# Optimization experiments

Measured on AMD Instinct MI355X. Metric: run time of the kernel, lower is better.

## Reference

```python
import jax, jax.numpy as jnp
import numpy as np

B, C, D, Hh, W = 2, 320, 4, 16, 16
N = D * Hh * W          # 1024 nodes
NH = 8                  # num_heads
DH = C // NH            # 40
L = 2                   # num_layers
A, EPD = 16, 64         # da_prior tokens, encode_prior_dim
EDGE_SCALE = 32 ** -0.5 # GraphEdgeFeature dim_head=32
SCALE = DH ** -0.5
EPS = 1e-5


def _ln(x, g, b):
    m = x.mean(-1, keepdims=True)
    v = ((x - m) ** 2).mean(-1, keepdims=True)
    return (x - m) * jax.lax.rsqrt(v + EPS) * g + b


def setup_inputs() -> dict:
    key = jax.random.key(0)
    ks = jax.random.split(key, 16)
    std = 0.02 / np.sqrt(L)
    inp = {
        'x': jax.random.normal(ks[0], (B, C, D, Hh, W), jnp.float32),
        'da_prior': jax.random.normal(ks[1], (B, A, EPD), jnp.float32),
        # GraphEdgeFeature.to_qk (no bias), init std 0.02/sqrt(24)
        'qk_w': jax.random.normal(ks[2], (2 * C, C), jnp.float32) * (0.02 / np.sqrt(24)),
        # fc_prior
        'fcp_w': jax.random.normal(ks[3], (C, EPD), jnp.float32) * 0.02,
        'fcp_b': jnp.zeros((C,), jnp.float32),
        # per-layer (stacked over L)
        'ln1_g': jnp.ones((L, C), jnp.float32),
        'ln1_b': jnp.zeros((L, C), jnp.float32),
        'gln_g': jnp.ones((L, C), jnp.float32),
        'gln_b': jnp.zeros((L, C), jnp.float32),
        'qkv_w': jax.random.normal(ks[4], (L, 3 * C, C), jnp.float32) * std,
        'qkv_b': jnp.zeros((L, 3 * C), jnp.float32),
        'proj_w': jax.random.normal(ks[5], (L, C, C), jnp.float32) * std,
        'proj_b': jnp.zeros((L, C), jnp.float32),
        # expand Conv2d(1, NH, 1): weight [NH], bias [NH]
        'exp_w': jax.random.normal(ks[6], (L, NH), jnp.float32),
        'exp_b': jnp.zeros((L, NH), jnp.float32),
        # reduce Conv2d(NH, 1, 1): weight [NH], bias scalar
        'red_w': jax.random.normal(ks[7], (L, NH), jnp.float32) / np.sqrt(NH),
        'red_b': jnp.zeros((L,), jnp.float32),
    }
    return inp


def _forward(x, da_prior, qk_w, fcp_w, fcp_b, ln1_g, ln1_b, gln_g, gln_b,
             qkv_w, qkv_b, proj_w, proj_b, exp_w, exp_b, red_w, red_b):
    node = x.reshape(B, C, N)                       # [B,C,N]
    # ---- GraphEdgeFeature: full-dim QK attention over nodes ----
    xt = node.transpose(0, 2, 1)                    # [B,N,C]
    qk = xt @ qk_w.T                                # [B,N,2C]
    q_e, k_e = jnp.split(qk, 2, axis=-1)
    edge = jax.nn.softmax(jnp.einsum('bqc,bkc->bqk', q_e, k_e) * EDGE_SCALE, axis=-1)  # [B,N,N]
    # ---- fc_prior ----
    da = da_prior @ fcp_w.T + fcp_b                 # [B,A,C]
    s = da.sum(axis=1)                              # [B,C] (sum over 'a' in einsum bnc,bca->bnc)
    for l in range(L):
        # block norm1 over channel dim
        nt = _ln(node.transpose(0, 2, 1), ln1_g[l], ln1_b[l])   # [B,N,C]
        # torch.einsum('bnn,bnc->bnc') takes the DIAGONAL of edge
        diag = jnp.diagonal(edge, axis1=1, axis2=2)             # [B,N]
        node2 = diag[:, :, None] * nt * s[:, None, :] + nt      # [B,N,C]
        y = _ln(node2, gln_g[l], gln_b[l])
        qkv = (y @ qkv_w[l].T + qkv_b[l]).reshape(B, N, 3, NH, DH)
        qkv = qkv.transpose(2, 0, 3, 1, 4)                      # [3,B,H,N,DH]
        q, k, v = qkv[0], qkv[1], qkv[2]
        attn = jnp.einsum('bhnd,bhmd->bhnm', q, k) * SCALE
        attn = attn + edge[:, None] * exp_w[l][None, :, None, None] + exp_b[l][None, :, None, None]
        a = jax.nn.softmax(attn, axis=-1)                       # [B,H,N,N]
        node_out = jnp.einsum('bhnm,bhmd->bhnd', a, v).transpose(0, 2, 1, 3).reshape(B, N, C)
        edge_new = jnp.einsum('bhnm,h->bnm', a + attn, red_w[l]) + red_b[l]  # [B,N,N]
        ws = jax.nn.softmax(edge_new, axis=-1)
        wsum = (ws * edge_new).sum(-1)                          # [B,N]
        node_out = node_out + wsum[:, :, None]                  # fc=Identity, broadcast
        node_out = node_out @ proj_w[l].T + proj_b[l]
        node = node_out.transpose(0, 2, 1)                      # [B,C,N]
        edge = edge + edge_new
    return node.reshape(B, C, D, Hh, W)


def reference(x, da_prior, qk_w, fcp_w, fcp_b, ln1_g, ln1_b, gln_g, gln_b,
              qkv_w, qkv_b, proj_w, proj_b, exp_w, exp_b, red_w, red_b):
    return _forward(x, da_prior, qk_w, fcp_w, fcp_b, ln1_g, ln1_b, gln_g, gln_b,
                    qkv_w, qkv_b, proj_w, proj_b, exp_w, exp_b, red_w, red_b)
```

## Files before the change

kernel.cpp:

```cpp
#include <hip/hip_runtime.h>
#include <math.h>

#define EDGE_SCALE 0.17677669529663687f
#define ATT_SCALE  0.15811388300841897f
#define LN_EPS 1e-5f

typedef __attribute__((ext_vector_type(8))) short bf8;
typedef __attribute__((ext_vector_type(4))) float f32x4;

__device__ __forceinline__ f32x4 mfma16(bf8 a, bf8 b, f32x4 c) {
  return __builtin_amdgcn_mfma_f32_16x16x32_bf16(a, b, c, 0, 0, 0);
}
__device__ __forceinline__ unsigned short f2bf(float f) {
  union { float f; unsigned u; } v; v.f = f;
  unsigned r = v.u + 0x7FFF + ((v.u >> 16) & 1);
  return (unsigned short)(r >> 16);
}
__device__ __forceinline__ float bf2f(unsigned short h) {
  union { unsigned u; float f; } v; v.u = ((unsigned)h) << 16;
  return v.f;
}
__device__ __forceinline__ float wave_max(float v) {
  #pragma unroll
  for (int o = 32; o > 0; o >>= 1) v = fmaxf(v, __shfl_xor(v, o));
  return v;
}
__device__ __forceinline__ float wave_sum(float v) {
  #pragma unroll
  for (int o = 32; o > 0; o >>= 1) v += __shfl_xor(v, o);
  return v;
}

__global__ __launch_bounds__(256) void k_trans(const float* __restrict__ x,
    float* __restrict__ node, unsigned short* __restrict__ nodebf) {
  __shared__ float tile[32][33];
  const int b = blockIdx.z;
  const int n0 = blockIdx.x * 32, c0 = blockIdx.y * 32;
  const int tx = threadIdx.x & 31, ty = threadIdx.x >> 5;
  #pragma unroll
  for (int k = 0; k < 4; ++k) {
    int c = c0 + ty + 8 * k;
    tile[ty + 8 * k][tx] = x[((size_t)b * 320 + c) * 1024 + n0 + tx];
  }
  __syncthreads();
  #pragma unroll
  for (int k = 0; k < 4; ++k) {
    int n = n0 + ty + 8 * k;
    float v = tile[tx][ty + 8 * k];
    size_t idx = ((size_t)b * 1024 + n) * 320 + c0 + tx;
    node[idx] = v;
    nodebf[idx] = f2bf(v);
  }
}

__global__ __launch_bounds__(320) void k_svec(const float* __restrict__ da,
    const float* __restrict__ fw, const float* __restrict__ fb, float* __restrict__ sv) {
  __shared__ float ds[64];
  const int b = blockIdx.x, t = threadIdx.x;
  if (t < 64) {
    float a = 0.f;
    #pragma unroll
    for (int i = 0; i < 16; ++i) a += da[b * 1024 + i * 64 + t];
    ds[t] = a;
  }
  __syncthreads();
  if (t < 320) {
    float acc = 16.f * fb[t];
    #pragma unroll
    for (int e = 0; e < 64; ++e) acc = fmaf(ds[e], fw[t * 64 + e], acc);
    sv[b * 320 + t] = acc;
  }
}

__global__ void k_wcvt(const float* __restrict__ a, int na,
                       const float* __restrict__ b, int nb,
                       const float* __restrict__ c, int nc,
                       unsigned short* __restrict__ out) {
  int tot = na + nb + nc;
  for (int i = blockIdx.x * blockDim.x + threadIdx.x; i < tot; i += gridDim.x * blockDim.x) {
    float v = (i < na) ? a[i] : ((i < na + nb) ? b[i - na] : c[i - na - nb]);
    out[i] = f2bf(v);
  }
}

__global__ void k_zero(float4* __restrict__ p) {
  p[blockIdx.x * blockDim.x + threadIdx.x] = make_float4(0.f, 0.f, 0.f, 0.f);
}

__global__ __launch_bounds__(256, 4) void k_mgemm(
    const unsigned short* __restrict__ A, const unsigned short* __restrict__ W,
    const float* __restrict__ bias, void* p0, void* p1, void* p2, int mode) {
  const int t = threadIdx.x, w = t >> 6, lane = t & 63;
  const int q16 = lane >> 4, l16 = lane & 15;
  const int rt = blockIdx.x * 64, jt = blockIdx.y * 64;
  f32x4 acc[4];
  #pragma unroll
  for (int i = 0; i < 4; ++i)
    #pragma unroll
    for (int j = 0; j < 4; ++j) acc[i][j] = 0.f;
  const unsigned short* ap = A + (size_t)(rt + 16 * w + l16) * 320 + q16 * 8;
  const unsigned short* wp = W + (size_t)(jt + l16) * 320 + q16 * 8;
  for (int kc = 0; kc < 10; ++kc) {
    bf8 af = *(const bf8*)(ap + kc * 32);
    #pragma unroll
    for (int ct = 0; ct < 4; ++ct) {
      bf8 bf = *(const bf8*)(wp + (size_t)ct * 16 * 320 + kc * 32);
      acc[ct] = mfma16(af, bf, acc[ct]);
    }
  }
  #pragma unroll
  for (int ct = 0; ct < 4; ++ct) {
    int col = jt + ct * 16 + l16;
    float bv = bias ? bias[col] : 0.f;
    #pragma unroll
    for (int r = 0; r < 4; ++r) {
      int row = rt + 16 * w + q16 * 4 + r;
      int b = row >> 10, n = row & 1023;
      float v = acc[ct][r] + bv;
      if (mode == 0) {
        ((float*)p0)[(size_t)row * 320 + col] = v;
      } else if (mode == 1) {
        if (col < 320) ((unsigned short*)p0)[(size_t)row * 320 + col] = f2bf(v);
        else           ((unsigned short*)p1)[(size_t)row * 320 + col - 320] = f2bf(v);
      } else if (mode == 2) {
        int part = col / 320, rem = col % 320;
        int h = rem / 40, d = rem % 40;
        size_t bh = (size_t)b * 8 + h;
        if (part == 0)      ((unsigned short*)p0)[(bh * 1024 + n) * 64 + d] = f2bf(v);
        else if (part == 1) ((unsigned short*)p1)[(bh * 1024 + n) * 64 + d] = f2bf(v);
        else                ((unsigned short*)p2)[(bh * 48 + d) * 1024 + n] = f2bf(v);
      } else {
        ((float*)p0)[((size_t)b * 320 + col) * 1024 + n] = v;
      }
    }
  }
}

__global__ __launch_bounds__(256, 2) void k_edge2(
    const unsigned short* __restrict__ qe, const unsigned short* __restrict__ ke,
    float* __restrict__ edge) {
  __shared__ float redm[4][16], reds[4][16];
  const int t = threadIdx.x, w = t >> 6, lane = t & 63;
  const int q16 = lane >> 4, l16 = lane & 15;
  const int b = blockIdx.y, n0 = blockIdx.x * 16;
  const unsigned short* qp = qe + ((size_t)b * 1024 + n0 + l16) * 320 + q16 * 8;
  bf8 af[10];
  #pragma unroll
  for (int kc = 0; kc < 10; ++kc) af[kc] = *(const bf8*)(qp + kc * 32);
  f32x4 acc[16];
  #pragma unroll
  for (int i = 0; i < 16; ++i)
    #pragma unroll
    for (int j = 0; j < 4; ++j) acc[i][j] = 0.f;
  const unsigned short* kp = ke + ((size_t)b * 1024 + w * 256 + l16) * 320 + q16 * 8;
  #pragma unroll
  for (int tt = 0; tt < 16; ++tt) {
    const unsigned short* kpt = kp + (size_t)tt * 16 * 320;
    #pragma unroll
    for (int kc = 0; kc < 10; ++kc) {
      bf8 bf = *(const bf8*)(kpt + kc * 32);
      acc[tt] = mfma16(af[kc], bf, acc[tt]);
    }
  }
  float pm[4] = {-3.4e38f, -3.4e38f, -3.4e38f, -3.4e38f};
  #pragma unroll
  for (int tt = 0; tt < 16; ++tt)
    #pragma unroll
    for (int r = 0; r < 4; ++r) {
      acc[tt][r] *= EDGE_SCALE;
      pm[r] = fmaxf(pm[r], acc[tt][r]);
    }
  #pragma unroll
  for (int r = 0; r < 4; ++r)
    #pragma unroll
    for (int o = 1; o <= 8; o <<= 1) pm[r] = fmaxf(pm[r], __shfl_xor(pm[r], o));
  if (l16 == 0) {
    #pragma unroll
    for (int r = 0; r < 4; ++r) redm[w][q16 * 4 + r] = pm[r];
  }
  __syncthreads();
  float m[4], ps[4] = {0.f, 0.f, 0.f, 0.f};
  #pragma unroll
  for (int r = 0; r < 4; ++r)
    m[r] = fmaxf(fmaxf(redm[0][q16 * 4 + r], redm[1][q16 * 4 + r]),
                 fmaxf(redm[2][q16 * 4 + r], redm[3][q16 * 4 + r]));
  #pragma unroll
  for (int tt = 0; tt < 16; ++tt)
    #pragma unroll
    for (int r = 0; r < 4; ++r) ps[r] += __expf(acc[tt][r] - m[r]);
  #pragma unroll
  for (int r = 0; r < 4; ++r)
    #pragma unroll
    for (int o = 1; o <= 8; o <<= 1) ps[r] += __shfl_xor(ps[r], o);
  if (l16 == 0) {
    #pragma unroll
    for (int r = 0; r < 4; ++r) reds[w][q16 * 4 + r] = ps[r];
  }
  __syncthreads();
  float inv[4];
  #pragma unroll
  for (int r = 0; r < 4; ++r)
    inv[r] = 1.f / (reds[0][q16 * 4 + r] + reds[1][q16 * 4 + r] +
                    reds[2][q16 * 4 + r] + reds[3][q16 * 4 + r]);
  float* ep = edge + ((size_t)b * 1024 + n0) * 1024 + w * 256 + l16;
  #pragma unroll
  for (int tt = 0; tt < 16; ++tt)
    #pragma unroll
    for (int r = 0; r < 4; ++r)
      ep[(size_t)(q16 * 4 + r) * 1024 + tt * 16] = __expf(acc[tt][r] - m[r]) * inv[r];
}

__global__ __launch_bounds__(256) void k_ln(const float* __restrict__ node,
    const float* __restrict__ edge, const float* __restrict__ sv,
    const float* __restrict__ g1, const float* __restrict__ b1,
    const float* __restrict__ g2, const float* __restrict__ b2,
    unsigned short* __restrict__ y) {
  const int w = threadIdx.x >> 6, lane = threadIdx.x & 63;
  const int row = blockIdx.x * 4 + w;
  const int b = row >> 10, n = row & 1023;
  const float* xr = node + (size_t)row * 320;
  float x[5];
  #pragma unroll
  for (int i = 0; i < 5; ++i) x[i] = xr[lane + 64 * i];
  float s = x[0] + x[1] + x[2] + x[3] + x[4];
  float mean = wave_sum(s) * (1.f / 320.f);
  float v = 0.f;
  #pragma unroll
  for (int i = 0; i < 5; ++i) { float d = x[i] - mean; v += d * d; }
  float rstd = rsqrtf(wave_sum(v) * (1.f / 320.f) + LN_EPS);
  float diag = edge[(size_t)row * 1024 + n];
  float n2[5];
  #pragma unroll
  for (int i = 0; i < 5; ++i) {
    int c = lane + 64 * i;
    float nt = (x[i] - mean) * rstd * g1[c] + b1[c];
    n2[i] = diag * nt * sv[b * 320 + c] + nt;
  }
  s = n2[0] + n2[1] + n2[2] + n2[3] + n2[4];
  float mean2 = wave_sum(s) * (1.f / 320.f);
  v = 0.f;
  #pragma unroll
  for (int i = 0; i < 5; ++i) { float d = n2[i] - mean2; v += d * d; }
  float rstd2 = rsqrtf(wave_sum(v) * (1.f / 320.f) + LN_EPS);
  unsigned short* yr = y + (size_t)row * 320;
  #pragma unroll
  for (int i = 0; i < 5; ++i) {
    int c = lane + 64 * i;
    yr[c] = f2bf((n2[i] - mean2) * rstd2 * g2[c] + b2[c]);
  }
}

__global__ __launch_bounds__(256, 3) void k_score(
    const unsigned short* __restrict__ qbf, const unsigned short* __restrict__ kbf,
    const unsigned short* __restrict__ vtb, const float* __restrict__ edge,
    unsigned short* __restrict__ thbuf, float* __restrict__ att,
    const float* __restrict__ ew, const float* __restrict__ eb,
    const float* __restrict__ rw) {
  __shared__ unsigned short a_lds[64][16][20];
  __shared__ float ored[4][3][16][17];
  __shared__ float redm[4][16], reds[4][16];
  const int t = threadIdx.x, w = t >> 6, lane = t & 63;
  const int q16 = lane >> 4, l16 = lane & 15;
  const int n0 = blockIdx.x * 16, h = blockIdx.y, b = blockIdx.z;
  const size_t bh = (size_t)b * 8 + h;
  const unsigned short* qp = qbf + (bh * 1024 + n0 + l16) * 64 + q16 * 8;
  bf8 af0 = *(const bf8*)(qp);
  bf8 af1 = *(const bf8*)(qp + 32);
  f32x4 acc[16];
  #pragma unroll
  for (int i = 0; i < 16; ++i)
    #pragma unroll
    for (int j = 0; j < 4; ++j) acc[i][j] = 0.f;
  const unsigned short* kp = kbf + (bh * 1024 + (size_t)w * 256 + l16) * 64 + q16 * 8;
  #pragma unroll
  for (int tt = 0; tt < 16; ++tt) {
    const unsigned short* kpt = kp + (size_t)tt * 16 * 64;
    bf8 b0 = *(const bf8*)(kpt);
    bf8 b1 = *(const bf8*)(kpt + 32);
    acc[tt] = mfma16(af0, b0, acc[tt]);
    acc[tt] = mfma16(af1, b1, acc[tt]);
  }
  const float ewh = ew[h], ebh = eb[h], rwh = rw[h];
  const float* ep = edge + ((size_t)b * 1024 + n0 + q16 * 4) * 1024 + w * 256 + l16;
  #pragma unroll
  for (int tt = 0; tt < 16; ++tt)
    #pragma unroll
    for (int r = 0; r < 4; ++r) {
      float ev = ep[(size_t)r * 1024 + tt * 16];
      acc[tt][r] = fmaf(acc[tt][r], ATT_SCALE, fmaf(ev, ewh, ebh));
    }
  float pm[4] = {-3.4e38f, -3.4e38f, -3.4e38f, -3.4e38f};
  #pragma unroll
  for (int tt = 0; tt < 16; ++tt)
    #pragma unroll
    for (int r = 0; r < 4; ++r) pm[r] = fmaxf(pm[r], acc[tt][r]);
  #pragma unroll
  for (int r = 0; r < 4; ++r)
    #pragma unroll
    for (int o = 1; o <= 8; o <<= 1) pm[r] = fmaxf(pm[r], __shfl_xor(pm[r], o));
  if (l16 == 0) {
    #pragma unroll
    for (int r = 0; r < 4; ++r) redm[w][q16 * 4 + r] = pm[r];
  }
  __syncthreads();
  float m[4], ps[4] = {0.f, 0.f, 0.f, 0.f};
  #pragma unroll
  for (int r = 0; r < 4; ++r)
    m[r] = fmaxf(fmaxf(redm[0][q16 * 4 + r], redm[1][q16 * 4 + r]),
                 fmaxf(redm[2][q16 * 4 + r], redm[3][q16 * 4 + r]));
  #pragma unroll
  for (int tt = 0; tt < 16; ++tt)
    #pragma unroll
    for (int r = 0; r < 4; ++r) ps[r] += __expf(acc[tt][r] - m[r]);
  #pragma unroll
  for (int r = 0; r < 4; ++r)
    #pragma unroll
    for (int o = 1; o <= 8; o <<= 1) ps[r] += __shfl_xor(ps[r], o);
  if (l16 == 0) {
    #pragma unroll
    for (int r = 0; r < 4; ++r) reds[w][q16 * 4 + r] = ps[r];
  }
  __syncthreads();
  float inv[4];
  #pragma unroll
  for (int r = 0; r < 4; ++r)
    inv[r] = 1.f / (reds[0][q16 * 4 + r] + reds[1][q16 * 4 + r] +
                    reds[2][q16 * 4 + r] + reds[3][q16 * 4 + r]);
  unsigned short* tp = thbuf + (bh * 1024 + n0 + q16 * 4) * 1024 + w * 256 + l16;
  #pragma unroll
  for (int tt = 0; tt < 16; ++tt)
    #pragma unroll
    for (int r = 0; r < 4; ++r) {
      float e = __expf(acc[tt][r] - m[r]);
      float a = e * inv[r];
      a_lds[w * 16 + tt][q16 * 4 + r][l16] = f2bf(a);
      tp[(size_t)r * 1024 + tt * 16] = f2bf(rwh * (a + acc[tt][r]));
    }
  f32x4 oacc[3];
  #pragma unroll
  for (int i = 0; i < 3; ++i)
    #pragma unroll
    for (int j = 0; j < 4; ++j) oacc[i][j] = 0.f;
  #pragma unroll
  for (int kc8 = 0; kc8 < 8; ++kc8) {
    int kc = w * 8 + kc8;
    int g0 = kc * 32 + q16 * 8;
    const unsigned short* ap2 = &a_lds[g0 >> 4][l16][g0 & 15];
    short4 lo = *(const short4*)(ap2);
    short4 hi = *(const short4*)(ap2 + 4);
    bf8 afv = {lo.x, lo.y, lo.z, lo.w, hi.x, hi.y, hi.z, hi.w};
    const unsigned short* vp = vtb + (bh * 48 + l16) * 1024 + (size_t)kc * 32 + q16 * 8;
    #pragma unroll
    for (int nt = 0; nt < 3; ++nt) {
      bf8 bfv = *(const bf8*)(vp + (size_t)nt * 16 * 1024);
      oacc[nt] = mfma16(afv, bfv, oacc[nt]);
    }
  }
  #pragma unroll
  for (int nt = 0; nt < 3; ++nt)
    #pragma unroll
    for (int r = 0; r < 4; ++r) ored[w][nt][q16 * 4 + r][l16] = oacc[nt][r];
  __syncthreads();
  #pragma unroll
  for (int k = 0; k < 3; ++k) {
    int o = k * 256 + t;
    int nt = o >> 8, row = (o >> 4) & 15, col = o & 15;
    int dim = nt * 16 + col;
    float sum = ored[0][nt][row][col] + ored[1][nt][row][col] +
                ored[2][nt][row][col] + ored[3][nt][row][col];
    if (dim < 40)
      att[((size_t)b * 1024 + n0 + row) * 320 + h * 40 + dim] = sum;
  }
}

__global__ __launch_bounds__(256) void k_wsum(
    const unsigned short* __restrict__ thbuf, float* __restrict__ edge,
    const float* __restrict__ att, unsigned short* __restrict__ attbf,
    const float* __restrict__ rb) {
  const int w = threadIdx.x >> 6, lane = threadIdx.x & 63;
  const int row = blockIdx.x * 4 + w;
  const int b = row >> 10, n = row & 1023;
  const float rbv = rb[0];
  float tv[16];
  #pragma unroll
  for (int i = 0; i < 16; ++i) tv[i] = rbv;
  #pragma unroll 1
  for (int h = 0; h < 8; ++h) {
    const unsigned short* tph = thbuf + (((size_t)b * 8 + h) * 1024 + n) * 1024 + lane * 4;
    #pragma unroll
    for (int seg = 0; seg < 4; ++seg) {
      ushort4 u = *(const ushort4*)(tph + seg * 256);
      tv[seg * 4 + 0] += bf2f(u.x);
      tv[seg * 4 + 1] += bf2f(u.y);
      tv[seg * 4 + 2] += bf2f(u.z);
      tv[seg * 4 + 3] += bf2f(u.w);
    }
  }
  float4* erp = (float4*)(edge + ((size_t)b * 1024 + n) * 1024) + lane;
  #pragma unroll
  for (int seg = 0; seg < 4; ++seg) {
    float4 e = erp[seg * 64];
    e.x += tv[seg * 4 + 0]; e.y += tv[seg * 4 + 1];
    e.z += tv[seg * 4 + 2]; e.w += tv[seg * 4 + 3];
    erp[seg * 64] = e;
  }
  float mx = -3.4e38f;
  #pragma unroll
  for (int i = 0; i < 16; ++i) mx = fmaxf(mx, tv[i]);
  mx = wave_max(mx);
  float s = 0.f, num = 0.f;
  #pragma unroll
  for (int i = 0; i < 16; ++i) {
    float e = __expf(tv[i] - mx);
    s += e; num += e * tv[i];
  }
  s = wave_sum(s); num = wave_sum(num);
  const float wsum = num / s;
  const float* ar = att + (size_t)row * 320;
  unsigned short* ao = attbf + (size_t)row * 320;
  #pragma unroll
  for (int i = 0; i < 5; ++i) {
    int c = lane + 64 * i;
    ao[c] = f2bf(ar[c] + wsum);
  }
}

extern "C" void kernel_launch(void* const* d_in, const int* in_sizes, int n_in,
                              void* d_out, int out_size, void* d_ws, size_t ws_size,
                              hipStream_t stream) {
  const float* x      = (const float*)d_in[0];
  const float* da     = (const float*)d_in[1];
  const float* qk_w   = (const float*)d_in[2];
  const float* fcp_w  = (const float*)d_in[3];
  const float* fcp_b  = (const float*)d_in[4];
  const float* ln1_g  = (const float*)d_in[5];
  const float* ln1_b  = (const float*)d_in[6];
  const float* gln_g  = (const float*)d_in[7];
  const float* gln_b  = (const float*)d_in[8];
  const float* qkv_w  = (const float*)d_in[9];
  const float* qkv_b  = (const float*)d_in[10];
  const float* proj_w = (const float*)d_in[11];
  const float* proj_b = (const float*)d_in[12];
  const float* exp_w  = (const float*)d_in[13];
  const float* exp_b  = (const float*)d_in[14];
  const float* red_w  = (const float*)d_in[15];
  const float* red_b  = (const float*)d_in[16];
  float* ws = (float*)d_ws;
  float* node  = ws + 0;
  unsigned short* ybf   = (unsigned short*)(ws + 655360);
  float* attb  = ws + 983040;
  unsigned short* attbf = (unsigned short*)(ws + 1638400);
  float* edge  = ws + 1966080;
  float* svec  = ws + 4063232;
  unsigned short* nodebf = (unsigned short*)(ws + 4063872);
  unsigned short* qe   = (unsigned short*)(ws + 4391552);
  unsigned short* ke   = (unsigned short*)(ws + 4719232);
  unsigned short* qbf  = (unsigned short*)(ws + 5046912);
  unsigned short* kbf  = (unsigned short*)(ws + 5571200);
  unsigned short* vtb  = (unsigned short*)(ws + 6095488);
  unsigned short* wbf  = (unsigned short*)(ws + 6488704);
  unsigned short* thbuf= (unsigned short*)(ws + 7000704);
  float* out = (float*)d_out;
  unsigned short* qk_wb   = wbf;
  unsigned short* qkv_wb  = wbf + 204800;
  unsigned short* proj_wb = wbf + 819200;

  hipLaunchKernelGGL(k_trans, dim3(32, 10, 2), dim3(256), 0, stream, x, node, nodebf);
  hipLaunchKernelGGL(k_svec, dim3(2), dim3(320), 0, stream, da, fcp_w, fcp_b, svec);
  hipLaunchKernelGGL(k_wcvt, dim3(512), dim3(256), 0, stream,
                     qk_w, 204800, qkv_w, 614400, proj_w, 204800, wbf);
  hipLaunchKernelGGL(k_mgemm, dim3(32, 10), dim3(256), 0, stream,
                     nodebf, qk_wb, (const float*)nullptr, qe, ke, (void*)nullptr, 1);
  hipLaunchKernelGGL(k_edge2, dim3(64, 2), dim3(256), 0, stream, qe, ke, edge);
  for (int l = 0; l < 2; ++l) {
    hipLaunchKernelGGL(k_ln, dim3(512), dim3(256), 0, stream, node, edge, svec,
                       ln1_g + l * 320, ln1_b + l * 320, gln_g + l * 320, gln_b + l * 320, ybf);
    hipLaunchKernelGGL(k_zero, dim3(1024), dim3(256), 0, stream, (float4*)qbf);
    hipLaunchKernelGGL(k_mgemm, dim3(32, 15), dim3(256), 0, stream,
                       ybf, qkv_wb + (size_t)l * 307200, qkv_b + l * 960, qbf, kbf, vtb, 2);
    hipLaunchKernelGGL(k_score, dim3(64, 8, 2), dim3(256), 0, stream,
                       qbf, kbf, vtb, edge, thbuf, attb,
                       exp_w + l * 8, exp_b + l * 8, red_w + l * 8);
    hipLaunchKernelGGL(k_wsum, dim3(512), dim3(256), 0, stream,
                       thbuf, edge, attb, attbf, red_b + l);
    if (l == 0)
      hipLaunchKernelGGL(k_mgemm, dim3(32, 5), dim3(256), 0, stream,
                         attbf, proj_wb, proj_b, node, (void*)nullptr, (void*)nullptr, 0);
    else
      hipLaunchKernelGGL(k_mgemm, dim3(32, 5), dim3(256), 0, stream,
                         attbf, proj_wb + 102400, proj_b + 320, out,
                         (void*)nullptr, (void*)nullptr, 3);
  }
}
```

Measured before the change: 300.9 us.

## Coalesce GEMM epilogues via LDS, split edge softmax, drop zero-fill kernel

The GEMM epilogues for the V-transpose and the final NCDHW output are now staged through shared memory, so each thread writes contiguous float4 chunks instead of strided scalar stores. Q/K padding columns are zeroed inside the GEMM, which removes the separate zero-fill launch. The fused edge-attention kernel, which ran only 128 blocks, is replaced by a tiled score GEMM that fills the device with more blocks plus a row-softmax kernel; this adds a 2x1024x1024 fp32 round trip through a scratch buffer. k_score now pipelines its P·V MFMAs in groups with a smaller LDS footprint and writes thbuf coalesced, allowing higher occupancy.

```diff
diff --git a/kernel.cpp b/kernel.cpp
--- a/kernel.cpp
+++ b/kernel.cpp
@@ -83,13 +83,10 @@
   }
 }
 
-__global__ void k_zero(float4* __restrict__ p) {
-  p[blockIdx.x * blockDim.x + threadIdx.x] = make_float4(0.f, 0.f, 0.f, 0.f);
-}
-
 __global__ __launch_bounds__(256, 4) void k_mgemm(
     const unsigned short* __restrict__ A, const unsigned short* __restrict__ W,
     const float* __restrict__ bias, void* p0, void* p1, void* p2, int mode) {
+  __shared__ float smem[64 * 65];
   const int t = threadIdx.x, w = t >> 6, lane = t & 63;
   const int q16 = lane >> 4, l16 = lane & 15;
   const int rt = blockIdx.x * 64, jt = blockIdx.y * 64;
@@ -108,106 +105,145 @@
       acc[ct] = mfma16(af, bf, acc[ct]);
     }
   }
-  #pragma unroll
-  for (int ct = 0; ct < 4; ++ct) {
-    int col = jt + ct * 16 + l16;
-    float bv = bias ? bias[col] : 0.f;
-    #pragma unroll
-    for (int r = 0; r < 4; ++r) {
-      int row = rt + 16 * w + q16 * 4 + r;
-      int b = row >> 10, n = row & 1023;
-      float v = acc[ct][r] + bv;
-      if (mode == 0) {
-        ((float*)p0)[(size_t)row * 320 + col] = v;
-      } else if (mode == 1) {
-        if (col < 320) ((unsigned short*)p0)[(size_t)row * 320 + col] = f2bf(v);
-        else           ((unsigned short*)p1)[(size_t)row * 320 + col - 320] = f2bf(v);
-      } else if (mode == 2) {
-        int part = col / 320, rem = col % 320;
+  if (mode == 0 || mode == 1) {
+    #pragma unroll
+    for (int ct = 0; ct < 4; ++ct) {
+      int col = jt + ct * 16 + l16;
+      float bv = bias ? bias[col] : 0.f;
+      #pragma unroll
+      for (int r = 0; r < 4; ++r) {
+        int row = rt + 16 * w + q16 * 4 + r;
+        float v = acc[ct][r] + bv;
+        if (mode == 0) {
+          ((float*)p0)[(size_t)row * 320 + col] = v;
+        } else {
+          if (col < 320) ((unsigned short*)p0)[(size_t)row * 320 + col] = f2bf(v);
+          else           ((unsigned short*)p1)[(size_t)row * 320 + col - 320] = f2bf(v);
+        }
+      }
+    }
+  } else if (mode == 2) {
+    const int part = jt / 320;
+    if (part < 2) {
+      unsigned short* dst = (unsigned short*)(part == 0 ? p0 : p1);
+      #pragma unroll
+      for (int ct = 0; ct < 4; ++ct) {
+        int col = jt + ct * 16 + l16;
+        float bv = bias[col];
+        int rem = col - part * 320;
         int h = rem / 40, d = rem % 40;
-        size_t bh = (size_t)b * 8 + h;
-        if (part == 0)      ((unsigned short*)p0)[(bh * 1024 + n) * 64 + d] = f2bf(v);
-        else if (part == 1) ((unsigned short*)p1)[(bh * 1024 + n) * 64 + d] = f2bf(v);
-        else                ((unsigned short*)p2)[(bh * 48 + d) * 1024 + n] = f2bf(v);
-      } else {
-        ((float*)p0)[((size_t)b * 320 + col) * 1024 + n] = v;
+        #pragma unroll
+        for (int r = 0; r < 4; ++r) {
+          int row = rt + 16 * w + q16 * 4 + r;
+          int b = row >> 10, n = row & 1023;
+          size_t base = (((size_t)b * 8 + h) * 1024 + n) * 64;
+          dst[base + d] = f2bf(acc[ct][r] + bv);
+          if (d < 24) dst[base + 40 + d] = 0;
+        }
       }
-    }
-  }
-}
-
-__global__ __launch_bounds__(256, 2) void k_edge2(
+    } else {
+      unsigned short* vt_t = (unsigned short*)smem;
+      #pragma unroll
+      for (int ct = 0; ct < 4; ++ct) {
+        int col = jt + ct * 16 + l16;
+        float bv = bias[col];
+        #pragma unroll
+        for (int r = 0; r < 4; ++r)
+          vt_t[(ct * 16 + l16) * 72 + 16 * w + q16 * 4 + r] = f2bf(acc[ct][r] + bv);
+      }
+      __syncthreads();
+      const int cl = t >> 2, seg = t & 3;
+      int rem = (jt - 640) + cl;
+      int h = rem / 40, d = rem % 40;
+      int b = rt >> 10, n = (rt & 1023) + seg * 16;
+      const float4* lp = (const float4*)&vt_t[cl * 72 + seg * 16];
+      float4 a0 = lp[0], a1 = lp[1];
+      float4* gp = (float4*)((unsigned short*)p2 +
+                             (((size_t)b * 8 + h) * 48 + d) * 1024 + n);
+      gp[0] = a0; gp[1] = a1;
+    }
+  } else {
+    #pragma unroll
+    for (int ct = 0; ct < 4; ++ct) {
+      int col = jt + ct * 16 + l16;
+      float bv = bias[col];
+      #pragma unroll
+      for (int r = 0; r < 4; ++r)
+        smem[(16 * w + q16 * 4 + r) * 65 + ct * 16 + l16] = acc[ct][r] + bv;
+    }
+    __syncthreads();
+    const int cl = t >> 2, seg = t & 3;
+    int b = rt >> 10, n = (rt & 1023) + seg * 16;
+    float* orow = (float*)p0 + ((size_t)b * 320 + jt + cl) * 1024 + n;
+    #pragma unroll
+    for (int i2 = 0; i2 < 4; ++i2) {
+      float4 vv;
+      vv.x = smem[(seg * 16 + i2 * 4 + 0) * 65 + cl];
+      vv.y = smem[(seg * 16 + i2 * 4 + 1) * 65 + cl];
+      vv.z = smem[(seg * 16 + i2 * 4 + 2) * 65 + cl];
+      vv.w = smem[(seg * 16 + i2 * 4 + 3) * 65 + cl];
+      ((float4*)orow)[i2] = vv;
+    }
+  }
+}
+
+__global__ __launch_bounds__(256, 4) void k_sgemm(
     const unsigned short* __restrict__ qe, const unsigned short* __restrict__ ke,
-    float* __restrict__ edge) {
-  __shared__ float redm[4][16], reds[4][16];
+    float* __restrict__ S) {
   const int t = threadIdx.x, w = t >> 6, lane = t & 63;
   const int q16 = lane >> 4, l16 = lane & 15;
-  const int b = blockIdx.y, n0 = blockIdx.x * 16;
-  const unsigned short* qp = qe + ((size_t)b * 1024 + n0 + l16) * 320 + q16 * 8;
-  bf8 af[10];
-  #pragma unroll
-  for (int kc = 0; kc < 10; ++kc) af[kc] = *(const bf8*)(qp + kc * 32);
-  f32x4 acc[16];
-  #pragma unroll
-  for (int i = 0; i < 16; ++i)
+  const int rt = blockIdx.x * 64, jt = blockIdx.y * 64, b = blockIdx.z;
+  const unsigned short* A = qe + (size_t)b * 1024 * 320;
+  const unsigned short* W = ke + (size_t)b * 1024 * 320;
+  f32x4 acc[4];
+  #pragma unroll
+  for (int i = 0; i < 4; ++i)
     #pragma unroll
     for (int j = 0; j < 4; ++j) acc[i][j] = 0.f;
-  const unsigned short* kp = ke + ((size_t)b * 1024 + w * 256 + l16) * 320 + q16 * 8;
-  #pragma unroll
-  for (int tt = 0; tt < 16; ++tt) {
-    const unsigned short* kpt = kp + (size_t)tt * 16 * 320;
-    #pragma unroll
-    for (int kc = 0; kc < 10; ++kc) {
-      bf8 bf = *(const bf8*)(kpt + kc * 32);
-      acc[tt] = mfma16(af[kc], bf, acc[tt]);
-    }
-  }
-  float pm[4] = {-3.4e38f, -3.4e38f, -3.4e38f, -3.4e38f};
-  #pragma unroll
-  for (int tt = 0; tt < 16; ++tt)
-    #pragma unroll
-    for (int r = 0; r < 4; ++r) {
-      acc[tt][r] *= EDGE_SCALE;
-      pm[r] = fmaxf(pm[r], acc[tt][r]);
-    }
-  #pragma unroll
-  for (int r = 0; r < 4; ++r)
-    #pragma unroll
-    for (int o = 1; o <= 8; o <<= 1) pm[r] = fmaxf(pm[r], __shfl_xor(pm[r], o));
-  if (l16 == 0) {
-    #pragma unroll
-    for (int r = 0; r < 4; ++r) redm[w][q16 * 4 + r] = pm[r];
-  }
-  __syncthreads();
-  float m[4], ps[4] = {0.f, 0.f, 0.f, 0.f};
-  #pragma unroll
-  for (int r = 0; r < 4; ++r)
-    m[r] = fmaxf(fmaxf(redm[0][q16 * 4 + r], redm[1][q16 * 4 + r]),
-                 fmaxf(redm[2][q16 * 4 + r], redm[3][q16 * 4 + r]));
-  #pragma unroll
-  for (int tt = 0; tt < 16; ++tt)
-    #pragma unroll
-    for (int r = 0; r < 4; ++r) ps[r] += __expf(acc[tt][r] - m[r]);
-  #pragma unroll
-  for (int r = 0; r < 4; ++r)
-    #pragma unroll
-    for (int o = 1; o <= 8; o <<= 1) ps[r] += __shfl_xor(ps[r], o);
-  if (l16 == 0) {
-    #pragma unroll
-    for (int r = 0; r < 4; ++r) reds[w][q16 * 4 + r] = ps[r];
-  }
-  __syncthreads();
-  float inv[4];
-  #pragma unroll
-  for (int r = 0; r < 4; ++r)
-    inv[r] = 1.f / (reds[0][q16 * 4 + r] + reds[1][q16 * 4 + r] +
-                    reds[2][q16 * 4 + r] + reds[3][q16 * 4 + r]);
-  float* ep = edge + ((size_t)b * 1024 + n0) * 1024 + w * 256 + l16;
-  #pragma unroll
-  for (int tt = 0; tt < 16; ++tt)
+  const unsigned short* ap = A + (size_t)(rt + 16 * w + l16) * 320 + q16 * 8;
+  const unsigned short* wp = W + (size_t)(jt + l16) * 320 + q16 * 8;
+  for (int kc = 0; kc < 10; ++kc) {
+    bf8 af = *(const bf8*)(ap + kc * 32);
+    #pragma unroll
+    for (int ct = 0; ct < 4; ++ct) {
+      bf8 bf = *(const bf8*)(wp + (size_t)ct * 16 * 320 + kc * 32);
+      acc[ct] = mfma16(af, bf, acc[ct]);
+    }
+  }
+  #pragma unroll
+  for (int ct = 0; ct < 4; ++ct)
     #pragma unroll
     for (int r = 0; r < 4; ++r)
-      ep[(size_t)(q16 * 4 + r) * 1024 + tt * 16] = __expf(acc[tt][r] - m[r]) * inv[r];
+      S[((size_t)b * 1024 + rt + 16 * w + q16 * 4 + r) * 1024 + jt + ct * 16 + l16] =
+          acc[ct][r] * EDGE_SCALE;
+}
+
+__global__ __launch_bounds__(256) void k_smax(const float* __restrict__ S,
+                                              float* __restrict__ edge) {
+  const int w = threadIdx.x >> 6, lane = threadIdx.x & 63;
+  const int row = blockIdx.x * 4 + w;
+  const float4* sp = (const float4*)(S + (size_t)row * 1024) + lane;
+  float4 v[4];
+  #pragma unroll
+  for (int i = 0; i < 4; ++i) v[i] = sp[i * 64];
+  float mx = -3.4e38f;
+  #pragma unroll
+  for (int i = 0; i < 4; ++i)
+    mx = fmaxf(mx, fmaxf(fmaxf(v[i].x, v[i].y), fmaxf(v[i].z, v[i].w)));
+  mx = wave_max(mx);
+  float s = 0.f;
+  #pragma unroll
+  for (int i = 0; i < 4; ++i) {
+    v[i].x = __expf(v[i].x - mx); v[i].y = __expf(v[i].y - mx);
+    v[i].z = __expf(v[i].z - mx); v[i].w = __expf(v[i].w - mx);
+    s += v[i].x + v[i].y + v[i].z + v[i].w;
+  }
+  s = wave_sum(s);
+  float inv = 1.f / s;
+  float4* ep = (float4*)(edge + (size_t)row * 1024) + lane;
+  #pragma unroll
+  for (int i = 0; i < 4; ++i)
+    ep[i * 64] = make_float4(v[i].x * inv, v[i].y * inv, v[i].z * inv, v[i].w * inv);
 }
 
 __global__ __launch_bounds__(256) void k_ln(const float* __restrict__ node,
@@ -250,13 +286,14 @@
   }
 }
 
-__global__ __launch_bounds__(256, 3) void k_score(
+__global__ __launch_bounds__(256, 4) void k_score(
     const unsigned short* __restrict__ qbf, const unsigned short* __restrict__ kbf,
     const unsigned short* __restrict__ vtb, const float* __restrict__ edge,
     unsigned short* __restrict__ thbuf, float* __restrict__ att,
     const float* __restrict__ ew, const float* __restrict__ eb,
     const float* __restrict__ rw) {
-  __shared__ unsigned short a_lds[64][16][20];
+  __shared__ unsigned short a_lds[4][4][16][20];
+  __shared__ unsigned short th_lds[4][16][72];
   __shared__ float ored[4][3][16][17];
   __shared__ float redm[4][16], reds[4][16];
   const int t = threadIdx.x, w = t >> 6, lane = t & 63;
@@ -326,34 +363,45 @@
   for (int r = 0; r < 4; ++r)
     inv[r] = 1.f / (reds[0][q16 * 4 + r] + reds[1][q16 * 4 + r] +
                     reds[2][q16 * 4 + r] + reds[3][q16 * 4 + r]);
-  unsigned short* tp = thbuf + (bh * 1024 + n0 + q16 * 4) * 1024 + w * 256 + l16;
-  #pragma unroll
-  for (int tt = 0; tt < 16; ++tt)
-    #pragma unroll
-    for (int r = 0; r < 4; ++r) {
-      float e = __expf(acc[tt][r] - m[r]);
-      float a = e * inv[r];
-      a_lds[w * 16 + tt][q16 * 4 + r][l16] = f2bf(a);
-      tp[(size_t)r * 1024 + tt * 16] = f2bf(rwh * (a + acc[tt][r]));
-    }
   f32x4 oacc[3];
   #pragma unroll
   for (int i = 0; i < 3; ++i)
     #pragma unroll
     for (int j = 0; j < 4; ++j) oacc[i][j] = 0.f;
-  #pragma unroll
-  for (int kc8 = 0; kc8 < 8; ++kc8) {
-    int kc = w * 8 + kc8;
-    int g0 = kc * 32 + q16 * 8;
-    const unsigned short* ap2 = &a_lds[g0 >> 4][l16][g0 & 15];
-    short4 lo = *(const short4*)(ap2);
-    short4 hi = *(const short4*)(ap2 + 4);
-    bf8 afv = {lo.x, lo.y, lo.z, lo.w, hi.x, hi.y, hi.z, hi.w};
-    const unsigned short* vp = vtb + (bh * 48 + l16) * 1024 + (size_t)kc * 32 + q16 * 8;
-    #pragma unroll
-    for (int nt = 0; nt < 3; ++nt) {
-      bf8 bfv = *(const bf8*)(vp + (size_t)nt * 16 * 1024);
-      oacc[nt] = mfma16(afv, bfv, oacc[nt]);
+  unsigned short* tbase = thbuf + (bh * 1024 + n0) * 1024 + w * 256;
+  const int trow = lane >> 2, tc4 = lane & 3;
+  #pragma unroll
+  for (int g = 0; g < 4; ++g) {
+    #pragma unroll
+    for (int ti = 0; ti < 4; ++ti) {
+      int tt = g * 4 + ti;
+      #pragma unroll
+      for (int r = 0; r < 4; ++r) {
+        float e = __expf(acc[tt][r] - m[r]);
+        float a = e * inv[r];
+        a_lds[w][ti][q16 * 4 + r][l16] = f2bf(a);
+        th_lds[w][q16 * 4 + r][ti * 16 + l16] = f2bf(rwh * (a + acc[tt][r]));
+      }
+    }
+    #pragma unroll
+    for (int kk = 0; kk < 2; ++kk) {
+      const unsigned short* ap2 = &a_lds[w][kk * 2 + (q16 >> 1)][l16][(q16 & 1) * 8];
+      short4 lo = *(const short4*)(ap2);
+      short4 hi = *(const short4*)(ap2 + 4);
+      bf8 afv = {lo.x, lo.y, lo.z, lo.w, hi.x, hi.y, hi.z, hi.w};
+      int kc = w * 8 + g * 2 + kk;
+      const unsigned short* vp = vtb + (bh * 48 + l16) * 1024 + (size_t)kc * 32 + q16 * 8;
+      #pragma unroll
+      for (int nt = 0; nt < 3; ++nt) {
+        bf8 bfv = *(const bf8*)(vp + (size_t)nt * 16 * 1024);
+        oacc[nt] = mfma16(afv, bfv, oacc[nt]);
+      }
+    }
+    {
+      const float4* lp = (const float4*)&th_lds[w][trow][tc4 * 16];
+      float4 v0 = lp[0], v1 = lp[1];
+      float4* gp = (float4*)(tbase + (size_t)trow * 1024 + g * 64 + tc4 * 16);
+      gp[0] = v0; gp[1] = v1;
     }
   }
   #pragma unroll
@@ -460,6 +508,7 @@
   unsigned short* vtb  = (unsigned short*)(ws + 6095488);
   unsigned short* wbf  = (unsigned short*)(ws + 6488704);
   unsigned short* thbuf= (unsigned short*)(ws + 7000704);
+  float* sbuf = ws + 15389312;
   float* out = (float*)d_out;
   unsigned short* qk_wb   = wbf;
   unsigned short* qkv_wb  = wbf + 204800;
@@ -471,11 +520,11 @@
                      qk_w, 204800, qkv_w, 614400, proj_w, 204800, wbf);
   hipLaunchKernelGGL(k_mgemm, dim3(32, 10), dim3(256), 0, stream,
                      nodebf, qk_wb, (const float*)nullptr, qe, ke, (void*)nullptr, 1);
-  hipLaunchKernelGGL(k_edge2, dim3(64, 2), dim3(256), 0, stream, qe, ke, edge);
+  hipLaunchKernelGGL(k_sgemm, dim3(16, 16, 2), dim3(256), 0, stream, qe, ke, sbuf);
+  hipLaunchKernelGGL(k_smax, dim3(512), dim3(256), 0, stream, sbuf, edge);
   for (int l = 0; l < 2; ++l) {
     hipLaunchKernelGGL(k_ln, dim3(512), dim3(256), 0, stream, node, edge, svec,
                        ln1_g + l * 320, ln1_b + l * 320, gln_g + l * 320, gln_b + l * 320, ybf);
-    hipLaunchKernelGGL(k_zero, dim3(1024), dim3(256), 0, stream, (float4*)qbf);
     hipLaunchKernelGGL(k_mgemm, dim3(32, 15), dim3(256), 0, stream,
                        ybf, qkv_wb + (size_t)l * 307200, qkv_b + l * 960, qbf, kbf, vtb, 2);
     hipLaunchKernelGGL(k_score, dim3(64, 8, 2), dim3(256), 0, stream,
```

Result: faster. 293.5 us (-2.4%).
